# Kernel optimization log

Measured on AMD Instinct MI355X. Metric: run time of the kernel, lower is better.

## Reference

```python
import jax, jax.numpy as jnp
import numpy as np

N, E, G = 50000, 800000, 64          # nodes, edges, graphs in batch
F, HG, HL = 64, 128, 128             # node feat, graph hidden, lin hidden
AVG_LOG = float(np.log(9.0))         # from deg histogram [0]*8+[1]: log(8+1)


def setup_inputs() -> dict:
    key = jax.random.key(0)
    ks = jax.random.split(key, 24)
    def w(k, shape):
        return 0.1 * jax.random.normal(k, shape, jnp.float32)
    return {
        "x": jax.random.normal(ks[0], (N, F), jnp.float32),
        "edge_index": jax.random.randint(ks[1], (2, E), 0, N),
        "edge_attr": jax.random.normal(ks[2], (E, 1), jnp.float32),
        "batch": jnp.sort(jax.random.randint(ks[3], (N,), 0, G)),
        # PNAConv params (towers=1, pre_layers=1, post_layers=1, edge_dim=1)
        "W_edge": w(ks[4], (1, F)),      "b_edge": w(ks[5], (F,)),
        "W_pre": w(ks[6], (3 * F, F)),   "b_pre": w(ks[7], (F,)),
        "W_post": w(ks[8], (13 * F, HG)), "b_post": w(ks[9], (HG,)),
        "W_lin": w(ks[10], (HG, HG)),    "b_lin": w(ks[11], (HG,)),
        # bn1 / fc2 / bn2
        "g1": jnp.ones((HG,)), "be1": jnp.zeros((HG,)),
        "W2": w(ks[12], (HG, HL)), "b2": w(ks[13], (HL,)),
        "g2": jnp.ones((HL,)), "be2": jnp.zeros((HL,)),
        # one resnet block: fc/bn/fc/bn
        "Wr1": w(ks[14], (HL, HL)), "br1": w(ks[15], (HL,)),
        "gr1": jnp.ones((HL,)), "ber1": jnp.zeros((HL,)),
        "Wr2": w(ks[16], (HL, HL)), "br2": w(ks[17], (HL,)),
        "gr2": jnp.ones((HL,)), "ber2": jnp.zeros((HL,)),
        "W_out": w(ks[18], (HL, 1)), "b_out": w(ks[19], (1,)),
    }


def _bn(z, g, b):
    # BatchNorm1d, training mode: biased batch stats, eps=1e-5
    mu = z.mean(0)
    var = ((z - mu) ** 2).mean(0)
    return (z - mu) * jax.lax.rsqrt(var + 1e-5) * g + b


def _pna(x, edge_index, edge_attr, W_edge, b_edge, W_pre, b_pre,
         W_post, b_post, W_lin, b_lin):
    src, dst = edge_index[0], edge_index[1]  # messages flow j->i, aggregate at dst
    e = edge_attr @ W_edge + b_edge                               # [E, F]
    m = jnp.concatenate([x[dst], x[src], e], -1) @ W_pre + b_pre  # [E, F]
    ones_e = jnp.ones((m.shape[0],), m.dtype)
    cnt = jax.ops.segment_sum(ones_e, dst, N)                     # in-degree
    cnt1 = jnp.maximum(cnt, 1.0)
    mean = jax.ops.segment_sum(m, dst, N) / cnt1[:, None]
    mean2 = jax.ops.segment_sum(m * m, dst, N) / cnt1[:, None]
    std = jnp.sqrt(jax.nn.relu(mean2 - mean * mean) + 1e-5)
    has = (cnt > 0)[:, None]
    mn = jnp.where(has, jax.ops.segment_min(m, dst, N), 0.0)
    mx = jnp.where(has, jax.ops.segment_max(m, dst, N), 0.0)
    agg = jnp.concatenate([mean, mn, mx, std], -1)                # [N, 4F]
    amp = (jnp.log(cnt1 + 1.0) / AVG_LOG)[:, None]                # amplification scaler
    out = jnp.concatenate([agg, agg * amp, agg / amp], -1)        # [N, 12F]
    out = jnp.concatenate([x, out], -1) @ W_post + b_post         # [N, HG]
    return out @ W_lin + b_lin                                    # [N, HG]


def reference(x, edge_index, edge_attr, batch,
              W_edge, b_edge, W_pre, b_pre, W_post, b_post, W_lin, b_lin,
              g1, be1, W2, b2, g2, be2,
              Wr1, br1, gr1, ber1, Wr2, br2, gr2, ber2,
              W_out, b_out):
    h = _pna(x, edge_index, edge_attr, W_edge, b_edge, W_pre, b_pre,
             W_post, b_post, W_lin, b_lin)
    # global_mean_pool over graphs
    gc = jnp.maximum(jax.ops.segment_sum(jnp.ones((h.shape[0],), h.dtype), batch, G), 1.0)
    z = jax.ops.segment_sum(h, batch, G) / gc[:, None]            # [G, HG]
    z = jax.nn.relu(_bn(z, g1, be1))
    z = jax.nn.relu(_bn(z @ W2 + b2, g2, be2))
    r = z
    z = jax.nn.relu(_bn(z @ Wr1 + br1, gr1, ber1))
    z = jax.nn.relu(_bn(z @ Wr2 + br2, gr2, ber2) + r)
    return z @ W_out + b_out                                      # [G, 1]
```

## Files before the change

kernel.cpp:

```cpp
#include <hip/hip_runtime.h>
#include <hip/hip_bf16.h>

using bf16 = __hip_bfloat16;

#define F 64
#define HG 128
#define HL 128
#define AVG_LOG_INV 0.45511961331341866f
#define BSH 5
#define BNODES 32
#define BCAP 1024
#define BTILE 8192
#define NBMAX 1664

typedef short short8 __attribute__((ext_vector_type(8)));
typedef float floatx4 __attribute__((ext_vector_type(4)));

__device__ __forceinline__ float b2f(bf16 v) { return __bfloat162float(v); }
__device__ __forceinline__ bf16 f2b(float v) { return __float2bfloat16(v); }
__device__ __forceinline__ short f2bs(float v) { bf16 h = f2b(v); return *(short*)&h; }

__device__ __forceinline__ unsigned packbf2(float x, float y) {
    bf16 a = f2b(x), b = f2b(y);
    unsigned short ua = *(unsigned short*)&a, ub = *(unsigned short*)&b;
    return ((unsigned)ub << 16) | (unsigned)ua;
}

__device__ __forceinline__ float wave_sum(float v) {
    #pragma unroll
    for (int m = 32; m > 0; m >>= 1) v += __shfl_xor(v, m);
    return v;
}

__global__ void k_ab_mfma(const float* __restrict__ x, const float* __restrict__ W_pre,
                          bf16* __restrict__ AB, int N,
                          int* __restrict__ gcur, float* __restrict__ gfeat,
                          int* __restrict__ gcnt, int NB, int GF, int G,
                          const float* __restrict__ W_edge, const float* __restrict__ b_edge,
                          const float* __restrict__ b_pre, float* __restrict__ uc) {
    int gtid = blockIdx.x * blockDim.x + threadIdx.x;
    int gstr = gridDim.x * blockDim.x;
    for (int i = gtid; i < GF; i += gstr) gfeat[i] = 0.f;
    for (int i = gtid; i < NB; i += gstr) gcur[i] = 0;
    for (int i = gtid; i < G; i += gstr) gcnt[i] = 0;
    if (blockIdx.x == 0 && threadIdx.x < 64) {
        int f = threadIdx.x;
        float u = 0.f, c = b_pre[f];
        for (int k = 0; k < 64; k++) {
            float w3 = W_pre[(128 + k) * 64 + f];
            u += W_edge[k] * w3;
            c += b_edge[k] * w3;
        }
        uc[f] = u; uc[64 + f] = c;
    }

    __shared__ unsigned short wt[128 * 72];
    for (int idx = threadIdx.x; idx < 8192; idx += 256) {
        int k = idx >> 7, m = idx & 127;
        float v = W_pre[((m & 64) + k) * 64 + (m & 63)];
        wt[m * 72 + k] = (unsigned short)f2bs(v);
    }
    __syncthreads();

    int lane = threadIdx.x & 63;
    int row = lane & 15, quad = lane >> 4;
    int w = (blockIdx.x * blockDim.x + threadIdx.x) >> 6;
    int nwaves = (gridDim.x * blockDim.x) >> 6;
    int ntiles = (N + 15) >> 4;

    for (int tile = w; tile < ntiles; tile += nwaves) {
        int m0 = tile << 4;
        int node_a = m0 + row; if (node_a >= N) node_a = N - 1;
        short8 a[2];
        #pragma unroll
        for (int h = 0; h < 2; h++) {
            const float* xp = x + (size_t)node_a * 64 + h * 32 + quad * 8;
            floatx4 v0 = *(const floatx4*)xp;
            floatx4 v1 = *(const floatx4*)(xp + 4);
            #pragma unroll
            for (int j = 0; j < 4; j++) { a[h][j] = f2bs(v0[j]); a[h][4 + j] = f2bs(v1[j]); }
        }
        #pragma unroll
        for (int t = 0; t < 8; t++) {
            int fbase = t * 16;
            floatx4 c = {0.f, 0.f, 0.f, 0.f};
            #pragma unroll
            for (int h = 0; h < 2; h++) {
                short8 b = *(const short8*)(wt + (fbase + row) * 72 + h * 32 + quad * 8);
                c = __builtin_amdgcn_mfma_f32_16x16x32_bf16(a[h], b, c, 0, 0, 0);
            }
            #pragma unroll
            for (int r = 0; r < 4; r++) {
                int node = m0 + quad * 4 + r;
                if (node < N) AB[(size_t)node * 128 + fbase + row] = f2b(c[r]);
            }
        }
    }
}

__global__ void k_bucket(const int* __restrict__ ei, const float* __restrict__ ea,
                         int* __restrict__ gcur, int2* __restrict__ gout,
                         int E, int NB) {
    __shared__ int2 recs[BTILE];
    __shared__ int hist[NBMAX], gst[NBMAX], lrk[NBMAX];
    int t = threadIdx.x;
    for (int b = t; b < NB; b += 1024) hist[b] = 0;
    __syncthreads();
    int base = blockIdx.x * BTILE;
    int lim = E - base; if (lim > BTILE) lim = BTILE;
    int nq = lim >> 2;
    const int4* src4 = (const int4*)(ei + base);
    const int4* dst4 = (const int4*)(ei + E + base);
    const float4* ea4 = (const float4*)(ea + base);
    for (int q = t; q < nq; q += 1024) {
        int4 s = src4[q], d = dst4[q];
        float4 v = ea4[q];
        int i = q * 4;
        recs[i]     = make_int2((d.x << 16) | s.x, __float_as_int(v.x));
        recs[i + 1] = make_int2((d.y << 16) | s.y, __float_as_int(v.y));
        recs[i + 2] = make_int2((d.z << 16) | s.z, __float_as_int(v.z));
        recs[i + 3] = make_int2((d.w << 16) | s.w, __float_as_int(v.w));
        atomicAdd(&hist[d.x >> BSH], 1);
        atomicAdd(&hist[d.y >> BSH], 1);
        atomicAdd(&hist[d.z >> BSH], 1);
        atomicAdd(&hist[d.w >> BSH], 1);
    }
    for (int i = (nq << 2) + t; i < lim; i += 1024) {
        int e = base + i;
        int src = ei[e], dst = ei[E + e];
        recs[i] = make_int2((dst << 16) | src, __float_as_int(ea[e]));
        atomicAdd(&hist[dst >> BSH], 1);
    }
    __syncthreads();
    for (int b = t; b < NB; b += 1024) {
        int h = hist[b];
        lrk[b] = 0;
        gst[b] = (h > 0) ? atomicAdd(&gcur[b], h) : 0;
    }
    __syncthreads();
    for (int i = t; i < lim; i += 1024) {
        int2 r = recs[i];
        int b = ((unsigned)r.x) >> (16 + BSH);
        int k = atomicAdd(&lrk[b], 1);
        int pos = gst[b] + k;
        if (pos < BCAP) gout[(size_t)b * BCAP + pos] = r;
    }
}

__global__ void k_edge(const bf16* __restrict__ AB, const int2* __restrict__ gout,
                       const int* __restrict__ gcur, const float* __restrict__ uc,
                       bf16* __restrict__ agg, float* __restrict__ ampv, int N) {
    __shared__ int2 recs[BCAP], sortd[BCAP];
    __shared__ int ncnt[BNODES], nofs[BNODES], nrank[BNODES];
    int t = threadIdx.x;
    int b = blockIdx.x;
    int nn = N - b * BNODES; if (nn > BNODES) nn = BNODES;
    int ecnt = gcur[b]; if (ecnt > BCAP) ecnt = BCAP;

    for (int i = t; i < ecnt; i += 512) recs[i] = gout[(size_t)b * BCAP + i];
    if (t < BNODES) { ncnt[t] = 0; nrank[t] = 0; }
    __syncthreads();
    for (int i = t; i < ecnt; i += 512)
        atomicAdd(&ncnt[((unsigned)recs[i].x >> 16) & (BNODES - 1)], 1);
    __syncthreads();
    if (t < BNODES) {
        int v = ncnt[t], inc = v;
        #pragma unroll
        for (int m = 1; m < BNODES; m <<= 1) { int u = __shfl_up(inc, m); if (t >= m) inc += u; }
        nofs[t] = inc - v;
    }
    __syncthreads();
    for (int i = t; i < ecnt; i += 512) {
        int2 r = recs[i];
        int nl = ((unsigned)r.x >> 16) & (BNODES - 1);
        int k = atomicAdd(&nrank[nl], 1);
        sortd[nofs[nl] + k] = r;
    }
    __syncthreads();

    int lane = t & 63, w = t >> 6;
    int half = lane & 31, hi32 = lane >> 5;
    float2 u2 = *(const float2*)(uc + 2 * half);
    float2 c2 = *(const float2*)(uc + 64 + 2 * half);

    for (int nl = w; nl < nn; nl += 8) {
        int n = b * BNODES + nl;
        int lo = nofs[nl], cnt = ncnt[nl], hi = lo + cnt;

        unsigned apack = *(const unsigned*)(AB + (size_t)n * 128 + 2 * half);
        float acx = __uint_as_float(apack << 16) + c2.x;
        float acy = __uint_as_float(apack & 0xffff0000u) + c2.y;

        float sx = 0.f, sy = 0.f, qx = 0.f, qy = 0.f;
        float mnx = 3.4e38f, mny = 3.4e38f, mxx = -3.4e38f, mxy = -3.4e38f;

        auto acc2 = [&](unsigned bp, float eav) {
            float bx = __uint_as_float(bp << 16);
            float by = __uint_as_float(bp & 0xffff0000u);
            float m0 = fmaf(eav, u2.x, acx) + bx;
            float m1 = fmaf(eav, u2.y, acy) + by;
            sx += m0; qx = fmaf(m0, m0, qx);
            sy += m1; qy = fmaf(m1, m1, qy);
            mnx = fminf(mnx, m0); mxx = fmaxf(mxx, m0);
            mny = fminf(mny, m1); mxy = fmaxf(mxy, m1);
        };
        auto gaddr = [&](int sn) {
            return (const unsigned*)(AB + (size_t)sn * 128 + 64 + 2 * half);
        };

        for (int base = lo; base < hi; base += 64) {
            int nb = hi - base; if (nb > 64) nb = 64;
            int2 rec = (lane < nb) ? sortd[base + lane] : make_int2(0, 0);
            int vsn = rec.x & 0xFFFF;
            float vea = __int_as_float(rec.y);
            int i = 0;
            for (; i + 8 <= nb; i += 8) {
                int sn0 = __shfl(vsn, i + hi32);
                int sn1 = __shfl(vsn, i + 2 + hi32);
                int sn2 = __shfl(vsn, i + 4 + hi32);
                int sn3 = __shfl(vsn, i + 6 + hi32);
                float e0 = __shfl(vea, i + hi32);
                float e1 = __shfl(vea, i + 2 + hi32);
                float e2 = __shfl(vea, i + 4 + hi32);
                float e3 = __shfl(vea, i + 6 + hi32);
                unsigned b0 = *gaddr(sn0);
                unsigned b1 = *gaddr(sn1);
                unsigned b2 = *gaddr(sn2);
                unsigned b3 = *gaddr(sn3);
                acc2(b0, e0); acc2(b1, e1); acc2(b2, e2); acc2(b3, e3);
            }
            for (; i + 2 <= nb; i += 2) {
                int   sn = __shfl(vsn, i + hi32);
                float ev = __shfl(vea, i + hi32);
                acc2(*gaddr(sn), ev);
            }
            if (i < nb) {
                int   sn = __shfl(vsn, i);
                float ev = __shfl(vea, i);
                unsigned bp = *gaddr(sn);
                if (hi32 == 0) acc2(bp, ev);
            }
        }
        sx += __shfl_xor(sx, 32); sy += __shfl_xor(sy, 32);
        qx += __shfl_xor(qx, 32); qy += __shfl_xor(qy, 32);
        mnx = fminf(mnx, __shfl_xor(mnx, 32)); mny = fminf(mny, __shfl_xor(mny, 32));
        mxx = fmaxf(mxx, __shfl_xor(mxx, 32)); mxy = fmaxf(mxy, __shfl_xor(mxy, 32));

        float c1 = (cnt > 0) ? (float)cnt : 1.f;
        float inv = 1.f / c1;
        float mex = sx * inv, mey = sy * inv;
        float vx = qx * inv - mex * mex; if (vx < 0.f) vx = 0.f;
        float vy = qy * inv - mey * mey; if (vy < 0.f) vy = 0.f;
        float sdx = sqrtf(vx + 1e-5f), sdy = sqrtf(vy + 1e-5f);
        if (cnt == 0) { mnx = mny = mxx = mxy = 0.f; }

        size_t ob = (size_t)n * 256 + 2 * half;
        if (hi32 == 0) {
            *(unsigned*)(agg + ob)       = packbf2(mex, mey);
            *(unsigned*)(agg + ob + 64)  = packbf2(mnx, mny);
        } else {
            *(unsigned*)(agg + ob + 128) = packbf2(mxx, mxy);
            *(unsigned*)(agg + ob + 192) = packbf2(sdx, sdy);
        }
        if (lane == 0) ampv[n] = logf(c1 + 1.f) * AVG_LOG_INV;
    }
}

__global__ void k_greduce2(const float* __restrict__ x, const bf16* __restrict__ agg,
                           const float* __restrict__ ampv, const int* __restrict__ batch,
                           float* __restrict__ gfeat, int* __restrict__ gcnt,
                           int N, int chunk) {
    int t = threadIdx.x;
    int lo = blockIdx.x * chunk;
    int hi = lo + chunk; if (hi > N) hi = N;
    if (lo >= hi) return;
    int curg = batch[lo];
    float s1 = 0.f, s2 = 0.f, s3 = 0.f, sx = 0.f;
    int cnt = 0;
    for (int n = lo; n < hi; n++) {
        int g = batch[n];
        if (g != curg) {
            float* gf = gfeat + (size_t)curg * 832;
            unsafeAtomicAdd(&gf[64 + t], s1);
            unsafeAtomicAdd(&gf[320 + t], s2);
            unsafeAtomicAdd(&gf[576 + t], s3);
            if (t < 64) unsafeAtomicAdd(&gf[t], sx);
            if (t == 0) atomicAdd(&gcnt[curg], cnt);
            s1 = s2 = s3 = sx = 0.f; cnt = 0; curg = g;
        }
        float amp = ampv[n];
        float av = b2f(agg[(size_t)n * 256 + t]);
        s1 += av; s2 += av * amp; s3 += av / amp;
        if (t < 64) sx += x[(size_t)n * 64 + t];
        cnt++;
    }
    float* gf = gfeat + (size_t)curg * 832;
    unsafeAtomicAdd(&gf[64 + t], s1);
    unsafeAtomicAdd(&gf[320 + t], s2);
    unsafeAtomicAdd(&gf[576 + t], s3);
    if (t < 64) unsafeAtomicAdd(&gf[t], sx);
    if (t == 0) atomicAdd(&gcnt[curg], cnt);
}

__global__ void k_post1(const float* __restrict__ gfeat, const int* __restrict__ gcnt,
                        const float* __restrict__ W_post, const float* __restrict__ b_post,
                        const float* __restrict__ W_lin, const float* __restrict__ b_lin,
                        float* __restrict__ Zin) {
    int g = blockIdx.x, j = threadIdx.x;
    __shared__ float feat[832];
    __shared__ float z1[128];
    int cg = gcnt[g];
    float r = 1.f / ((cg > 0) ? (float)cg : 1.f);
    for (int i = j; i < 832; i += 128) feat[i] = gfeat[(size_t)g * 832 + i] * r;
    __syncthreads();
    float acc = b_post[j];
    for (int k = 0; k < 832; k++) acc += feat[k] * W_post[k * 128 + j];
    z1[j] = acc;
    __syncthreads();
    float a2 = b_lin[j];
    for (int k = 0; k < 128; k++) a2 += z1[k] * W_lin[k * 128 + j];
    if (cg == 0) a2 = 0.f;
    Zin[g * 128 + j] = a2;
}

__global__ void k_mlpcol(const float* __restrict__ in, const float* __restrict__ W,
                         const float* __restrict__ bias,
                         const float* __restrict__ gamma, const float* __restrict__ beta,
                         const float* __restrict__ res,
                         const float* __restrict__ g_in, const float* __restrict__ be_in,
                         float* __restrict__ outp) {
    __shared__ float A[64 * 129];
    __shared__ float part[4 * 64];
    int t = threadIdx.x;
    int j = blockIdx.x;

    for (int i = t; i < 8192; i += 256) A[(i >> 7) * 129 + (i & 127)] = in[i];
    __syncthreads();

    if (g_in) {
        if (t < 128) {
            int c = t;
            float mu = 0.f;
            for (int r = 0; r < 64; r++) mu += A[r * 129 + c];
            mu *= (1.f / 64.f);
            float var = 0.f;
            for (int r = 0; r < 64; r++) { float d = A[r * 129 + c] - mu; var += d * d; }
            var *= (1.f / 64.f);
            float sc = rsqrtf(var + 1e-5f) * g_in[c], sh = be_in[c];
            for (int r = 0; r < 64; r++) {
                float v = (A[r * 129 + c] - mu) * sc + sh;
                A[r * 129 + c] = v > 0.f ? v : 0.f;
            }
        }
        __syncthreads();
    }

    int r = t & 63, q = t >> 6;
    float acc = 0.f;
    int k0 = q * 32;
    #pragma unroll
    for (int k = 0; k < 32; k++) acc += A[r * 129 + k0 + k] * W[(k0 + k) * 128 + j];
    part[q * 64 + r] = acc;
    __syncthreads();

    if (t < 64) {
        float v = part[t] + part[64 + t] + part[128 + t] + part[192 + t] + bias[j];
        float mu = wave_sum(v) * (1.f / 64.f);
        float d = v - mu;
        float var = wave_sum(d * d) * (1.f / 64.f);
        float o = d * rsqrtf(var + 1e-5f) * gamma[j] + beta[j];
        if (res) o += res[t * 128 + j];
        outp[t * 128 + j] = o > 0.f ? o : 0.f;
    }
}

__global__ void k_out(const float* __restrict__ z4, const float* __restrict__ W_out,
                      const float* b_out, float* __restrict__ out) {
    int g = threadIdx.x;
    float acc = b_out[0];
    for (int j = 0; j < 128; j++) acc += z4[g * 128 + j] * W_out[j];
    out[g] = acc;
}

extern "C" void kernel_launch(void* const* d_in, const int* in_sizes, int n_in,
                              void* d_out, int out_size, void* d_ws, size_t ws_size,
                              hipStream_t stream) {
    const float* x      = (const float*)d_in[0];
    const int*   ei     = (const int*)d_in[1];
    const float* ea     = (const float*)d_in[2];
    const int*   batch  = (const int*)d_in[3];
    const float* W_edge = (const float*)d_in[4];
    const float* b_edge = (const float*)d_in[5];
    const float* W_pre  = (const float*)d_in[6];
    const float* b_pre  = (const float*)d_in[7];
    const float* W_post = (const float*)d_in[8];
    const float* b_post = (const float*)d_in[9];
    const float* W_lin  = (const float*)d_in[10];
    const float* b_lin  = (const float*)d_in[11];
    const float* g1     = (const float*)d_in[12];
    const float* be1    = (const float*)d_in[13];
    const float* W2     = (const float*)d_in[14];
    const float* b2     = (const float*)d_in[15];
    const float* g2     = (const float*)d_in[16];
    const float* be2    = (const float*)d_in[17];
    const float* Wr1    = (const float*)d_in[18];
    const float* br1    = (const float*)d_in[19];
    const float* gr1    = (const float*)d_in[20];
    const float* ber1   = (const float*)d_in[21];
    const float* Wr2    = (const float*)d_in[22];
    const float* br2    = (const float*)d_in[23];
    const float* gr2    = (const float*)d_in[24];
    const float* ber2   = (const float*)d_in[25];
    const float* W_out  = (const float*)d_in[26];
    const float* b_out  = (const float*)d_in[27];
    float* out = (float*)d_out;

    const int N = in_sizes[0] / F;
    const int E = in_sizes[1] / 2;
    const int G = out_size;
    const int NB = (N + BNODES - 1) >> BSH;

    char* p = (char*)d_ws;
    auto alloc = [&](size_t nbytes) { void* r = p; p += (nbytes + 255) & ~(size_t)255; return r; };
    bf16*  AB     = (bf16*)alloc((size_t)N * 128 * sizeof(bf16));
    bf16*  agg    = (bf16*)alloc((size_t)N * 256 * sizeof(bf16));
    float* ampv   = (float*)alloc((size_t)N * sizeof(float));
    int*   gcur   = (int*)alloc((size_t)NB * sizeof(int));
    int2*  gout   = (int2*)alloc((size_t)NB * BCAP * sizeof(int2));
    float* uc     = (float*)alloc(128 * sizeof(float));
    float* gfeat  = (float*)alloc((size_t)G * 832 * sizeof(float));
    int*   gcnt   = (int*)alloc((size_t)G * sizeof(int));
    float* Zin    = (float*)alloc(64 * 128 * sizeof(float));
    float* z2b    = (float*)alloc(64 * 128 * sizeof(float));
    float* z3b    = (float*)alloc(64 * 128 * sizeof(float));
    float* z4b    = (float*)alloc(64 * 128 * sizeof(float));

    const int GF = G * 832;
    const int GRB = 1024;
    const int GRCH = (N + GRB - 1) / GRB;
    const int ABB = ((N + 15) / 16 + 3) / 4;
    const int NBT = (E + BTILE - 1) / BTILE;

    k_ab_mfma<<<ABB, 256, 0, stream>>>(x, W_pre, AB, N, gcur, gfeat, gcnt, NB, GF, G,
                                       W_edge, b_edge, b_pre, uc);
    k_bucket<<<NBT, 1024, 0, stream>>>(ei, ea, gcur, gout, E, NB);
    k_edge<<<NB, 512, 0, stream>>>(AB, gout, gcur, uc, agg, ampv, N);
    k_greduce2<<<GRB, 256, 0, stream>>>(x, agg, ampv, batch, gfeat, gcnt, N, GRCH);
    k_post1<<<G, 128, 0, stream>>>(gfeat, gcnt, W_post, b_post, W_lin, b_lin, Zin);
    k_mlpcol<<<HG, 256, 0, stream>>>(Zin, W2, b2, g2, be2, nullptr, g1, be1, z2b);
    k_mlpcol<<<HL, 256, 0, stream>>>(z2b, Wr1, br1, gr1, ber1, nullptr, nullptr, nullptr, z3b);
    k_mlpcol<<<HL, 256, 0, stream>>>(z3b, Wr2, br2, gr2, ber2, z2b, nullptr, nullptr, z4b);
    k_out<<<1, 64, 0, stream>>>(z4b, W_out, b_out, out);
}
```

Before: 238.2 us.

## Fuse per-graph aggregate pooling into edge kernel, drop agg intermediate buffer

The edge kernel now stages per-node aggregate stats in shared memory and reduces them directly into per-graph sums with global atomics, so the N×256 bf16 agg buffer and the ampv array are never written or reread. The old greduce kernel is cut down to pooling raw x features and node counts. This removes a large global write and read round trip. In exchange the edge kernel uses more shared memory, which may lower occupancy, and adds many more global float atomics (about six per column per graph segment per block).

Result: no change. 237.0 us (-0.5%).

```diff
diff --git a/kernel.cpp b/kernel.cpp
--- a/kernel.cpp
+++ b/kernel.cpp
@@ -149,16 +149,23 @@
 
 __global__ void k_edge(const bf16* __restrict__ AB, const int2* __restrict__ gout,
                        const int* __restrict__ gcur, const float* __restrict__ uc,
-                       bf16* __restrict__ agg, float* __restrict__ ampv, int N) {
+                       const int* __restrict__ batch, float* __restrict__ gfeat,
+                       int N) {
     __shared__ int2 recs[BCAP], sortd[BCAP];
     __shared__ int ncnt[BNODES], nofs[BNODES], nrank[BNODES];
+    __shared__ int gid[BNODES];
+    __shared__ unsigned lstat[BNODES][128];
+    __shared__ float lamp[BNODES], liamp[BNODES];
     int t = threadIdx.x;
     int b = blockIdx.x;
     int nn = N - b * BNODES; if (nn > BNODES) nn = BNODES;
     int ecnt = gcur[b]; if (ecnt > BCAP) ecnt = BCAP;
 
     for (int i = t; i < ecnt; i += 512) recs[i] = gout[(size_t)b * BCAP + i];
-    if (t < BNODES) { ncnt[t] = 0; nrank[t] = 0; }
+    if (t < BNODES) {
+        ncnt[t] = 0; nrank[t] = 0;
+        if (t < nn) gid[t] = batch[b * BNODES + t];
+    }
     __syncthreads();
     for (int i = t; i < ecnt; i += 512)
         atomicAdd(&ncnt[((unsigned)recs[i].x >> 16) & (BNODES - 1)], 1);
@@ -254,51 +261,76 @@
         float sdx = sqrtf(vx + 1e-5f), sdy = sqrtf(vy + 1e-5f);
         if (cnt == 0) { mnx = mny = mxx = mxy = 0.f; }
 
-        size_t ob = (size_t)n * 256 + 2 * half;
         if (hi32 == 0) {
-            *(unsigned*)(agg + ob)       = packbf2(mex, mey);
-            *(unsigned*)(agg + ob + 64)  = packbf2(mnx, mny);
+            lstat[nl][half]      = packbf2(mex, mey);
+            lstat[nl][32 + half] = packbf2(mnx, mny);
         } else {
-            *(unsigned*)(agg + ob + 128) = packbf2(mxx, mxy);
-            *(unsigned*)(agg + ob + 192) = packbf2(sdx, sdy);
-        }
-        if (lane == 0) ampv[n] = logf(c1 + 1.f) * AVG_LOG_INV;
-    }
-}
-
-__global__ void k_greduce2(const float* __restrict__ x, const bf16* __restrict__ agg,
-                           const float* __restrict__ ampv, const int* __restrict__ batch,
-                           float* __restrict__ gfeat, int* __restrict__ gcnt,
-                           int N, int chunk) {
+            lstat[nl][64 + half] = packbf2(mxx, mxy);
+            lstat[nl][96 + half] = packbf2(sdx, sdy);
+        }
+        if (lane == 0) {
+            float amp = logf(c1 + 1.f) * AVG_LOG_INV;
+            lamp[nl] = amp; liamp[nl] = 1.f / amp;
+        }
+    }
+    __syncthreads();
+
+    if (t < 128) {
+        int c = t;
+        int elem = ((c >> 5) << 6) + ((c & 31) << 1);
+        float s1x = 0.f, s1y = 0.f, s2x = 0.f, s2y = 0.f, s3x = 0.f, s3y = 0.f;
+        int cur = gid[0];
+        for (int nl = 0; nl < nn; nl++) {
+            int g = gid[nl];
+            if (g != cur) {
+                float* gf = gfeat + (size_t)cur * 832;
+                unsafeAtomicAdd(&gf[64 + elem], s1x);
+                unsafeAtomicAdd(&gf[65 + elem], s1y);
+                unsafeAtomicAdd(&gf[320 + elem], s2x);
+                unsafeAtomicAdd(&gf[321 + elem], s2y);
+                unsafeAtomicAdd(&gf[576 + elem], s3x);
+                unsafeAtomicAdd(&gf[577 + elem], s3y);
+                s1x = s1y = s2x = s2y = s3x = s3y = 0.f;
+                cur = g;
+            }
+            unsigned p = lstat[nl][c];
+            float bx = __uint_as_float(p << 16);
+            float by = __uint_as_float(p & 0xffff0000u);
+            float a = lamp[nl], ia = liamp[nl];
+            s1x += bx; s2x = fmaf(bx, a, s2x); s3x = fmaf(bx, ia, s3x);
+            s1y += by; s2y = fmaf(by, a, s2y); s3y = fmaf(by, ia, s3y);
+        }
+        float* gf = gfeat + (size_t)cur * 832;
+        unsafeAtomicAdd(&gf[64 + elem], s1x);
+        unsafeAtomicAdd(&gf[65 + elem], s1y);
+        unsafeAtomicAdd(&gf[320 + elem], s2x);
+        unsafeAtomicAdd(&gf[321 + elem], s2y);
+        unsafeAtomicAdd(&gf[576 + elem], s3x);
+        unsafeAtomicAdd(&gf[577 + elem], s3y);
+    }
+}
+
+__global__ void k_gx(const float* __restrict__ x, const int* __restrict__ batch,
+                     float* __restrict__ gfeat, int* __restrict__ gcnt,
+                     int N, int chunk) {
     int t = threadIdx.x;
     int lo = blockIdx.x * chunk;
     int hi = lo + chunk; if (hi > N) hi = N;
     if (lo >= hi) return;
     int curg = batch[lo];
-    float s1 = 0.f, s2 = 0.f, s3 = 0.f, sx = 0.f;
+    float sx = 0.f;
     int cnt = 0;
     for (int n = lo; n < hi; n++) {
         int g = batch[n];
         if (g != curg) {
-            float* gf = gfeat + (size_t)curg * 832;
-            unsafeAtomicAdd(&gf[64 + t], s1);
-            unsafeAtomicAdd(&gf[320 + t], s2);
-            unsafeAtomicAdd(&gf[576 + t], s3);
-            if (t < 64) unsafeAtomicAdd(&gf[t], sx);
+            unsafeAtomicAdd(&gfeat[(size_t)curg * 832 + t], sx);
             if (t == 0) atomicAdd(&gcnt[curg], cnt);
-            s1 = s2 = s3 = sx = 0.f; cnt = 0; curg = g;
-        }
-        float amp = ampv[n];
-        float av = b2f(agg[(size_t)n * 256 + t]);
-        s1 += av; s2 += av * amp; s3 += av / amp;
-        if (t < 64) sx += x[(size_t)n * 64 + t];
+            sx = 0.f; cnt = 0; curg = g;
+        }
+        sx += x[(size_t)n * 64 + t];
         cnt++;
     }
-    float* gf = gfeat + (size_t)curg * 832;
-    unsafeAtomicAdd(&gf[64 + t], s1);
-    unsafeAtomicAdd(&gf[320 + t], s2);
-    unsafeAtomicAdd(&gf[576 + t], s3);
-    if (t < 64) unsafeAtomicAdd(&gf[t], sx);
+    unsafeAtomicAdd(&gfeat[(size_t)curg * 832 + t], sx);
     if (t == 0) atomicAdd(&gcnt[curg], cnt);
 }
 
@@ -423,8 +455,6 @@
     char* p = (char*)d_ws;
     auto alloc = [&](size_t nbytes) { void* r = p; p += (nbytes + 255) & ~(size_t)255; return r; };
     bf16*  AB     = (bf16*)alloc((size_t)N * 128 * sizeof(bf16));
-    bf16*  agg    = (bf16*)alloc((size_t)N * 256 * sizeof(bf16));
-    float* ampv   = (float*)alloc((size_t)N * sizeof(float));
     int*   gcur   = (int*)alloc((size_t)NB * sizeof(int));
     int2*  gout   = (int2*)alloc((size_t)NB * BCAP * sizeof(int2));
     float* uc     = (float*)alloc(128 * sizeof(float));
@@ -436,16 +466,16 @@
     float* z4b    = (float*)alloc(64 * 128 * sizeof(float));
 
     const int GF = G * 832;
-    const int GRB = 1024;
-    const int GRCH = (N + GRB - 1) / GRB;
+    const int GXB = 2048;
+    const int GXCH = (N + GXB - 1) / GXB;
     const int ABB = ((N + 15) / 16 + 3) / 4;
     const int NBT = (E + BTILE - 1) / BTILE;
 
     k_ab_mfma<<<ABB, 256, 0, stream>>>(x, W_pre, AB, N, gcur, gfeat, gcnt, NB, GF, G,
                                        W_edge, b_edge, b_pre, uc);
     k_bucket<<<NBT, 1024, 0, stream>>>(ei, ea, gcur, gout, E, NB);
-    k_edge<<<NB, 512, 0, stream>>>(AB, gout, gcur, uc, agg, ampv, N);
-    k_greduce2<<<GRB, 256, 0, stream>>>(x, agg, ampv, batch, gfeat, gcnt, N, GRCH);
+    k_edge<<<NB, 512, 0, stream>>>(AB, gout, gcur, uc, batch, gfeat, N);
+    k_gx<<<GXB, 64, 0, stream>>>(x, batch, gfeat, gcnt, N, GXCH);
     k_post1<<<G, 128, 0, stream>>>(gfeat, gcnt, W_post, b_post, W_lin, b_lin, Zin);
     k_mlpcol<<<HG, 256, 0, stream>>>(Zin, W2, b2, g2, be2, nullptr, g1, be1, z2b);
     k_mlpcol<<<HL, 256, 0, stream>>>(z2b, Wr1, br1, gr1, ber1, nullptr, nullptr, nullptr, z3b);
```
